# Kernel tuning notes

Hardware: AMD Instinct MI355X
Metric: run time of the kernel (lower is better)

The kernel has to match this reference:

```python
import jax, jax.numpy as jnp
import numpy as np

D_MODEL = 1024
N_HEADS = 16
D_K = D_MODEL // N_HEADS
B, N_Q, N_KV = 2, 2048, 2048


def setup_inputs() -> dict:
    key = jax.random.key(0)
    ks = jax.random.split(key, 13)
    s = 1.0 / np.sqrt(D_MODEL)
    Q = jax.random.normal(ks[0], (B, N_Q, D_MODEL), dtype=jnp.float32)
    K = jax.random.normal(ks[1], (B, N_KV, D_MODEL), dtype=jnp.float32)
    V = jax.random.normal(ks[2], (B, N_KV, D_MODEL), dtype=jnp.float32)
    mask = jax.random.uniform(ks[3], (B, N_KV)) > 0.1
    mask = mask.at[:, 0].set(True)  # ensure at least one valid kv per batch
    Wq = jax.random.uniform(ks[4], (D_MODEL, D_MODEL), minval=-s, maxval=s)
    bq = jax.random.uniform(ks[5], (D_MODEL,), minval=-s, maxval=s)
    Wk = jax.random.uniform(ks[6], (D_MODEL, D_MODEL), minval=-s, maxval=s)
    bk = jax.random.uniform(ks[7], (D_MODEL,), minval=-s, maxval=s)
    Wv = jax.random.uniform(ks[8], (D_MODEL, D_MODEL), minval=-s, maxval=s)
    bv = jax.random.uniform(ks[9], (D_MODEL,), minval=-s, maxval=s)
    Wo = jax.random.uniform(ks[10], (D_MODEL, D_MODEL), minval=-s, maxval=s)
    bo = jax.random.uniform(ks[11], (D_MODEL,), minval=-s, maxval=s)
    return {"Q": Q, "K": K, "V": V, "mask": mask,
            "Wq": Wq, "bq": bq, "Wk": Wk, "bk": bk,
            "Wv": Wv, "bv": bv, "Wo": Wo, "bo": bo}


def reference(Q, K, V, mask, Wq, bq, Wk, bk, Wv, bv, Wo, bo):
    Bsz, nq, _ = Q.shape
    nkv = K.shape[1]
    # torch Linear: y = x @ W.T + b
    q = (Q @ Wq.T + bq).reshape(Bsz, nq, N_HEADS, D_K).transpose(0, 2, 1, 3)
    k = (K @ Wk.T + bk).reshape(Bsz, nkv, N_HEADS, D_K).transpose(0, 2, 1, 3)
    v = (V @ Wv.T + bv).reshape(Bsz, nkv, N_HEADS, D_K).transpose(0, 2, 1, 3)
    scores = jnp.einsum('bhqd,bhkd->bhqk', q, k) / jnp.sqrt(jnp.float32(D_K))
    scores = jnp.where(mask[:, None, None, :], scores, -jnp.inf)
    attn = jax.nn.softmax(scores, axis=-1)  # dropout p=0 (eval) -> identity
    out = jnp.einsum('bhqk,bhkd->bhqd', attn, v)
    out = out.transpose(0, 2, 1, 3).reshape(Bsz, nq, D_MODEL)
    return (out @ Wo.T + bo, attn)
```

## Files before the change

### kernel.cpp

```cpp
#include <hip/hip_runtime.h>
#include <math.h>

#define H 16
#define DK 64
#define NSEQ 2048
#define DM 1024
#define BSZ 2

typedef float f32x4 __attribute__((ext_vector_type(4)));
typedef short bf16x8 __attribute__((ext_vector_type(8)));
typedef unsigned short u16;
typedef unsigned long long u64;

__device__ __forceinline__ u16 f2bf(float f) {
    unsigned int u = __float_as_uint(f);
    u += 0x7fffu + ((u >> 16) & 1u);
    return (u16)(u >> 16);
}
__device__ __forceinline__ float bf2f(u16 h) {
    return __uint_as_float(((unsigned int)h) << 16);
}
__device__ __forceinline__ unsigned f2fp8(float v) {
    unsigned u = __float_as_uint(v);
    unsigned r = u + 0x7FFFFu + ((u >> 20) & 1u);
    unsigned byte = ((r >> 20) - 0x3C0u) & 0x7Fu;
    return v == 0.f ? 0u : byte;
}
__device__ __forceinline__ float fp82f(unsigned b) {
    return b ? __uint_as_float((b + 0x3C0u) << 20) : 0.f;
}

__global__ __launch_bounds__(256)
void cvt4_bf16(const float* __restrict__ s0, const float* __restrict__ s1,
               const float* __restrict__ s2, const float* __restrict__ s3,
               u16* __restrict__ dst) {
    const int sel = blockIdx.x >> 10;
    const float* s = sel == 0 ? s0 : sel == 1 ? s1 : sel == 2 ? s2 : s3;
    const int i = ((blockIdx.x & 1023) * 256 + threadIdx.x) * 4;
    float4 v = *(const float4*)(&s[i]);
    ushort4 o = make_ushort4(f2bf(v.x), f2bf(v.y), f2bf(v.z), f2bf(v.w));
    *(ushort4*)(&dst[(size_t)sel * DM * DM + i]) = o;
}

__global__ __launch_bounds__(1024, 4)
void gemm_qkv(const float* __restrict__ Qs_, const float* __restrict__ Ks_,
              const float* __restrict__ Vs_,
              const u16* __restrict__ Wqb, const u16* __restrict__ Wkb,
              const u16* __restrict__ Wvb,
              const float* __restrict__ bq, const float* __restrict__ bk,
              const float* __restrict__ bv,
              u16* __restrict__ qd, u16* __restrict__ kd, u16* __restrict__ vt) {
    __shared__ __align__(16) u16 At[64 * 1024];

    const int which = blockIdx.x >> 6;
    const int mblk  = blockIdx.x & 63;
    const float* A    = which == 0 ? Qs_ : which == 1 ? Ks_ : Vs_;
    const u16*   Wb   = which == 0 ? Wqb : which == 1 ? Wkb : Wvb;
    const float* bias = which == 0 ? bq  : which == 1 ? bk  : bv;

    const int tid  = threadIdx.x;
    const int lane = tid & 63;
    const int w    = tid >> 6;
    const int m0   = mblk * 64;

    {
        const int row = tid & 63;
        const int kg  = tid >> 6;
#pragma unroll
        for (int i = 0; i < 8; ++i) {
            int k = kg * 64 + i * 8;
            float4 a0 = *(const float4*)(&A[(size_t)(m0 + row) * 1024 + k]);
            float4 a1 = *(const float4*)(&A[(size_t)(m0 + row) * 1024 + k + 4]);
            bf16x8 pv;
            pv[0] = (short)f2bf(a0.x); pv[1] = (short)f2bf(a0.y);
            pv[2] = (short)f2bf(a0.z); pv[3] = (short)f2bf(a0.w);
            pv[4] = (short)f2bf(a1.x); pv[5] = (short)f2bf(a1.y);
            pv[6] = (short)f2bf(a1.z); pv[7] = (short)f2bf(a1.w);
            int slot = (kg * 8 + i) ^ (row & 7);
            *(bf16x8*)(&At[row * 1024 + slot * 8]) = pv;
        }
    }
    __syncthreads();

    const int fr = lane & 15;
    const int fg = lane >> 4;

    f32x4 acc[4][4];
#pragma unroll
    for (int rf = 0; rf < 4; ++rf)
#pragma unroll
        for (int ct = 0; ct < 4; ++ct) acc[rf][ct] = {0.f, 0.f, 0.f, 0.f};

    const int nbase = w * 64;
    for (int ks = 0; ks < 32; ++ks) {
        int slot = (ks * 4 + fg) ^ (fr & 7);
        bf16x8 aA[4];
#pragma unroll
        for (int rf = 0; rf < 4; ++rf)
            aA[rf] = *(const bf16x8*)(&At[(rf * 16 + fr) * 1024 + slot * 8]);
#pragma unroll
        for (int ct = 0; ct < 4; ++ct) {
            bf16x8 bB = *(const bf16x8*)(&Wb[(size_t)(nbase + ct * 16 + fr) * 1024 + ks * 32 + fg * 8]);
#pragma unroll
            for (int rf = 0; rf < 4; ++rf)
                acc[rf][ct] = __builtin_amdgcn_mfma_f32_16x16x32_bf16(aA[rf], bB, acc[rf][ct], 0, 0, 0);
        }
    }

    const int b = m0 >> 11;
    if (which == 2) {
#pragma unroll
        for (int ct = 0; ct < 4; ++ct) {
            int n = nbase + ct * 16 + fr;
            float bvv = bias[n];
            int hh = n >> 6, d = n & 63;
            size_t base = ((size_t)(b * H + hh)) * DK * NSEQ + (size_t)d * NSEQ;
#pragma unroll
            for (int rf = 0; rf < 4; ++rf) {
                int kv = (m0 & 2047) + rf * 16 + fg * 4;
                ushort4 pk = make_ushort4(f2bf(acc[rf][ct][0] + bvv), f2bf(acc[rf][ct][1] + bvv),
                                          f2bf(acc[rf][ct][2] + bvv), f2bf(acc[rf][ct][3] + bvv));
                *(ushort4*)(&vt[base + kv]) = pk;
            }
        }
    } else {
        u16* C = which == 0 ? qd : kd;
#pragma unroll
        for (int ct = 0; ct < 4; ++ct) {
            int n = nbase + ct * 16 + fr;
            float bvv = bias[n];
            int hh = n >> 6, d = n & 63;
#pragma unroll
            for (int rf = 0; rf < 4; ++rf)
#pragma unroll
                for (int reg = 0; reg < 4; ++reg) {
                    int nq = (m0 & 2047) + rf * 16 + fg * 4 + reg;
                    C[(((size_t)(b * H + hh)) * NSEQ + nq) * DK + d] = f2bf(acc[rf][ct][reg] + bvv);
                }
        }
    }
}

__global__ __launch_bounds__(512)
void gemm_out(const u16* __restrict__ Ab, const u16* __restrict__ Wb,
              const float* __restrict__ bias, float* __restrict__ Cdst) {
    __shared__ __align__(16) char smem[32 * 1028 * 4];
    u16* At = (u16*)smem;

    const int tid  = threadIdx.x;
    const int lane = tid & 63;
    const int w    = tid >> 6;
    const int m0   = blockIdx.x * 32;

    {
        const int row = tid & 31;
        const int kg  = tid >> 5;
#pragma unroll
        for (int i = 0; i < 8; ++i) {
            int k = kg * 64 + i * 8;
            bf16x8 pv = *(const bf16x8*)(&Ab[(size_t)(m0 + row) * 1024 + k]);
            int slot = (kg * 8 + i) ^ (row & 7);
            *(bf16x8*)(&At[row * 1024 + slot * 8]) = pv;
        }
    }
    __syncthreads();

    const int fr = lane & 15;
    const int fg = lane >> 4;

    f32x4 acc[2][8];
#pragma unroll
    for (int rf = 0; rf < 2; ++rf)
#pragma unroll
        for (int ct = 0; ct < 8; ++ct) acc[rf][ct] = {0.f, 0.f, 0.f, 0.f};

    const int nbase = w * 128;
    for (int ks = 0; ks < 32; ++ks) {
        int slot = (ks * 4 + fg) ^ (fr & 7);
        bf16x8 aA0 = *(const bf16x8*)(&At[(fr     ) * 1024 + slot * 8]);
        bf16x8 aA1 = *(const bf16x8*)(&At[(16 + fr) * 1024 + slot * 8]);
#pragma unroll
        for (int ct = 0; ct < 8; ++ct) {
            bf16x8 bB = *(const bf16x8*)(&Wb[(size_t)(nbase + ct * 16 + fr) * 1024 + ks * 32 + fg * 8]);
            acc[0][ct] = __builtin_amdgcn_mfma_f32_16x16x32_bf16(aA0, bB, acc[0][ct], 0, 0, 0);
            acc[1][ct] = __builtin_amdgcn_mfma_f32_16x16x32_bf16(aA1, bB, acc[1][ct], 0, 0, 0);
        }
    }

    __syncthreads();
    float* Ct = (float*)smem;
#pragma unroll
    for (int ct = 0; ct < 8; ++ct) {
        int n = nbase + ct * 16 + fr;
        float bvv = bias[n];
#pragma unroll
        for (int rf = 0; rf < 2; ++rf)
#pragma unroll
            for (int reg = 0; reg < 4; ++reg)
                Ct[(rf * 16 + fg * 4 + reg) * 1028 + n] = acc[rf][ct][reg] + bvv;
    }
    __syncthreads();
#pragma unroll
    for (int rr = 0; rr < 4; ++rr) {
        int row = w * 4 + rr;
#pragma unroll
        for (int seg = 0; seg < 4; ++seg) {
            int c = seg * 256 + lane * 4;
            f32x4 v = *(const f32x4*)(&Ct[row * 1028 + c]);
            *(f32x4*)(&Cdst[(size_t)(m0 + row) * 1024 + c]) = v;
        }
    }
}

__global__ __launch_bounds__(512, 4)
void attn_mfma(const u16* __restrict__ qb, const u16* __restrict__ kb,
               const u16* __restrict__ vt, const int* __restrict__ mask,
               float* __restrict__ attn, u16* __restrict__ ao) {
    __shared__ __align__(16) unsigned char Pband[32][2056];
    __shared__ unsigned Mbits[64];
    __shared__ float Sws[8][32];
    __shared__ float Sinv[32];

    const int tid  = threadIdx.x;
    const int lane = tid & 63;
    const int w    = tid >> 6;
    const int fr   = lane & 15;
    const int fg   = lane >> 4;

    const int bid = blockIdx.x;
    const int wg  = (bid & 7) * 256 + (bid >> 3);
    const int bh  = wg >> 6;
    const int qt  = wg & 63;
    const int b   = bh / H, h = bh % H;
    const int q0  = qt * 32;

    const u16* qh = qb + (size_t)bh * NSEQ * DK;
    const u16* kh = kb + (size_t)bh * NSEQ * DK;
    const u16* vh = vt + (size_t)bh * DK * NSEQ;

#pragma unroll
    for (int j = 0; j < 4; ++j) {
        int kv = j * 512 + w * 64 + lane;
        unsigned long long bal = __ballot(mask[b * NSEQ + kv] != 0);
        if (lane == 0) {
            Mbits[j * 16 + w * 2]     = (unsigned)bal;
            Mbits[j * 16 + w * 2 + 1] = (unsigned)(bal >> 32);
        }
    }

    bf16x8 aQ[2][2];
#pragma unroll
    for (int qs = 0; qs < 2; ++qs)
#pragma unroll
        for (int ks = 0; ks < 2; ++ks)
            aQ[qs][ks] = *(const bf16x8*)(&qh[(size_t)(q0 + qs * 16 + fr) * DK + ks * 32 + fg * 8]);

    const int slab = w * 32;

    __syncthreads();

    float sum[2] = {0.f, 0.f};
    f32x4 accO[2][4];
#pragma unroll
    for (int qs = 0; qs < 2; ++qs)
#pragma unroll
        for (int g = 0; g < 4; ++g) accO[qs][g] = {0.f, 0.f, 0.f, 0.f};
    const float lscale = 0.125f * 1.44269504089f;

    const int kvbSel = fg >> 1;
    const int srcA   = ((fg & 1) * 2) * 16 + fr;
    const int srcB   = srcA + 16;

    for (int st = 0; st < 8; ++st) {
        const int cb = st * 256;

        bf16x8 bV[4];
#pragma unroll
        for (int g = 0; g < 4; ++g)
            bV[g] = *(const bf16x8*)(&vh[(size_t)(g * 16 + fr) * NSEQ + cb + slab + fg * 8]);

        bf16x8 aK[2][2];
#pragma unroll
        for (int kvb = 0; kvb < 2; ++kvb)
#pragma unroll
            for (int ks = 0; ks < 2; ++ks)
                aK[kvb][ks] = *(const bf16x8*)(&kh[(size_t)(cb + slab + kvb * 16 + fr) * DK + ks * 32 + fg * 8]);

        __builtin_amdgcn_s_setprio(1);
        f32x4 s[2][2];
#pragma unroll
        for (int qs = 0; qs < 2; ++qs)
#pragma unroll
            for (int kvb = 0; kvb < 2; ++kvb) {
                s[qs][kvb] = {0.f, 0.f, 0.f, 0.f};
#pragma unroll
                for (int ks = 0; ks < 2; ++ks)
                    s[qs][kvb] = __builtin_amdgcn_mfma_f32_16x16x32_bf16(aK[kvb][ks], aQ[qs][ks], s[qs][kvb], 0, 0, 0);
            }
        __builtin_amdgcn_s_setprio(0);

        const unsigned word = Mbits[st * 8 + w];
        u64 pkll[2][2];
#pragma unroll
        for (int qs = 0; qs < 2; ++qs)
#pragma unroll
            for (int kvb = 0; kvb < 2; ++kvb) {
                float e[4];
                unsigned p8 = 0;
                u64 pb = 0;
#pragma unroll
                for (int reg = 0; reg < 4; ++reg) {
                    bool mm = (word >> (kvb * 16 + fg * 4 + reg)) & 1u;
                    e[reg] = mm ? exp2f(s[qs][kvb][reg] * lscale) : 0.f;
                    sum[qs] += e[reg];
                    p8 |= f2fp8(e[reg]) << (reg * 8);
                    pb |= (u64)f2bf(e[reg]) << (reg * 16);
                }
                pkll[qs][kvb] = pb;
                *(unsigned*)(&Pband[qs * 16 + fr][cb + slab + kvb * 16 + fg * 4]) = p8;
            }

        __builtin_amdgcn_s_setprio(1);
#pragma unroll
        for (int qs = 0; qs < 2; ++qs) {
            u64 tA0 = (u64)__shfl((long long)pkll[qs][0], srcA);
            u64 tA1 = (u64)__shfl((long long)pkll[qs][1], srcA);
            u64 tB0 = (u64)__shfl((long long)pkll[qs][0], srcB);
            u64 tB1 = (u64)__shfl((long long)pkll[qs][1], srcB);
            u64 lo = kvbSel ? tA1 : tA0;
            u64 hi = kvbSel ? tB1 : tB0;
            bf16x8 aP;
#pragma unroll
            for (int j = 0; j < 4; ++j) {
                aP[j]     = (short)(u16)(lo >> (j * 16));
                aP[4 + j] = (short)(u16)(hi >> (j * 16));
            }
#pragma unroll
            for (int g = 0; g < 4; ++g)
                accO[qs][g] = __builtin_amdgcn_mfma_f32_16x16x32_bf16(aP, bV[g], accO[qs][g], 0, 0, 0);
        }
        __builtin_amdgcn_s_setprio(0);
    }

#pragma unroll
    for (int off = 16; off < 64; off <<= 1) {
#pragma unroll
        for (int qs = 0; qs < 2; ++qs)
            sum[qs] += __shfl_xor(sum[qs], off);
    }
    if (fg == 0) {
#pragma unroll
        for (int qs = 0; qs < 2; ++qs)
            Sws[w][qs * 16 + fr] = sum[qs];
    }
    __syncthreads();
    if (tid < 32) {
        float s = 0.f;
#pragma unroll
        for (int wv = 0; wv < 8; ++wv) s += Sws[wv][tid];
        Sinv[tid] = 1.0f / s;
    }
    __syncthreads();

#pragma unroll
    for (int rr = 0; rr < 4; ++rr) {
        int row = w * 4 + rr;
        float inv = Sinv[row];
        float* dst = attn + ((size_t)bh * NSEQ + q0 + row) * NSEQ;
#pragma unroll
        for (int seg = 0; seg < 8; ++seg) {
            int c = seg * 256 + lane * 4;
            unsigned wq = *(const unsigned*)(&Pband[row][c]);
            f32x4 o = { fp82f( wq        & 0xFFu) * inv,
                        fp82f((wq >>  8) & 0xFFu) * inv,
                        fp82f((wq >> 16) & 0xFFu) * inv,
                        fp82f((wq >> 24) & 0xFFu) * inv };
            __builtin_nontemporal_store(o, (f32x4*)(&dst[c]));
        }
    }

    asm volatile("s_waitcnt lgkmcnt(0)" ::: "memory");
    __builtin_amdgcn_sched_barrier(0);
    __builtin_amdgcn_s_barrier();

    float* Of = (float*)Pband;
#pragma unroll
    for (int qs = 0; qs < 2; ++qs)
#pragma unroll
        for (int g = 0; g < 4; ++g)
#pragma unroll
            for (int reg = 0; reg < 4; ++reg)
                Of[(w * 32 + qs * 16 + fg * 4 + reg) * 64 + g * 16 + fr] = accO[qs][g][reg];
    __syncthreads();
    {
        int row = tid >> 4, cq = (tid & 15) * 4;
        f32x4 o = {0.f, 0.f, 0.f, 0.f};
#pragma unroll
        for (int wv = 0; wv < 8; ++wv)
            o += *(const f32x4*)(&Of[(wv * 32 + row) * 64 + cq]);
        float inv = Sinv[row];
        ushort4 st4 = make_ushort4(f2bf(o[0] * inv), f2bf(o[1] * inv),
                                   f2bf(o[2] * inv), f2bf(o[3] * inv));
        *(ushort4*)(&ao[((size_t)(b * NSEQ + q0 + row)) * DM + h * DK + cq]) = st4;
    }
}

extern "C" void kernel_launch(void* const* d_in, const int* in_sizes, int n_in,
                              void* d_out, int out_size, void* d_ws, size_t ws_size,
                              hipStream_t stream) {
    const float* Q    = (const float*)d_in[0];
    const float* K    = (const float*)d_in[1];
    const float* V    = (const float*)d_in[2];
    const int*   mask = (const int*)  d_in[3];
    const float* Wq   = (const float*)d_in[4];
    const float* bq   = (const float*)d_in[5];
    const float* Wk   = (const float*)d_in[6];
    const float* bk   = (const float*)d_in[7];
    const float* Wv   = (const float*)d_in[8];
    const float* bv   = (const float*)d_in[9];
    const float* Wo   = (const float*)d_in[10];
    const float* bo   = (const float*)d_in[11];

    float* out  = (float*)d_out;
    float* attn = out + (size_t)BSZ * NSEQ * DM;

    u16* Wqb = (u16*)d_ws;
    u16* Wkb = Wqb + (size_t)DM * DM;
    u16* Wvb = Wkb + (size_t)DM * DM;
    u16* Wob = Wvb + (size_t)DM * DM;
    u16* qbp = Wob + (size_t)DM * DM;
    u16* kbp = qbp + (size_t)BSZ * NSEQ * DM;
    u16* vbp = kbp + (size_t)BSZ * NSEQ * DM;
    u16* aob = vbp + (size_t)BSZ * NSEQ * DM;
    u16* vtb = aob + (size_t)BSZ * NSEQ * DM;

    cvt4_bf16<<<dim3(4096), dim3(256), 0, stream>>>(Wq, Wk, Wv, Wo, Wqb);

    gemm_qkv<<<dim3(192), dim3(1024), 0, stream>>>(Q, K, V, Wqb, Wkb, Wvb,
                                                   bq, bk, bv, qbp, kbp, vtb);

    attn_mfma<<<dim3(BSZ * H * (NSEQ / 32)), dim3(512), 0, stream>>>(qbp, kbp, vtb, mask, attn, aob);

    gemm_out<<<dim3(BSZ * NSEQ / 32), dim3(512), 0, stream>>>(aob, Wob, bo, out);
}
```

Baseline: 310.3 us.

## Prefetch next K tile and stage P through LDS instead of shuffles

Loads K fragments for the next kv step ahead of time (register double-buffering) so global load latency overlaps compute. It replaces the cross-lane shuffles that rebuild the bf16 P operand with a small per-wave LDS staging buffer, written and read back after an lgkmcnt wait. The loop is also split per query sub-tile so the two sub-tiles interleave. In exchange it uses more registers for the prefetched K, adds LDS traffic and a full lgkmcnt wait, and reuses the Stag buffer across the qs iterations without a barrier, relying on in-wave ordering.

```diff
diff --git a/kernel.cpp b/kernel.cpp
--- a/kernel.cpp
+++ b/kernel.cpp
@@ -217,6 +217,7 @@
                const u16* __restrict__ vt, const int* __restrict__ mask,
                float* __restrict__ attn, u16* __restrict__ ao) {
     __shared__ __align__(16) unsigned char Pband[32][2056];
+    __shared__ __align__(16) u16 Stag[8][16][40];
     __shared__ unsigned Mbits[64];
     __shared__ float Sws[8][32];
     __shared__ float Sinv[32];
@@ -267,9 +268,12 @@
         for (int g = 0; g < 4; ++g) accO[qs][g] = {0.f, 0.f, 0.f, 0.f};
     const float lscale = 0.125f * 1.44269504089f;
 
-    const int kvbSel = fg >> 1;
-    const int srcA   = ((fg & 1) * 2) * 16 + fr;
-    const int srcB   = srcA + 16;
+    bf16x8 aKc[2][2];
+#pragma unroll
+    for (int kvb = 0; kvb < 2; ++kvb)
+#pragma unroll
+        for (int ks = 0; ks < 2; ++ks)
+            aKc[kvb][ks] = *(const bf16x8*)(&kh[(size_t)(slab + kvb * 16 + fr) * DK + ks * 32 + fg * 8]);
 
     for (int st = 0; st < 8; ++st) {
         const int cb = st * 256;
@@ -279,67 +283,59 @@
         for (int g = 0; g < 4; ++g)
             bV[g] = *(const bf16x8*)(&vh[(size_t)(g * 16 + fr) * NSEQ + cb + slab + fg * 8]);
 
-        bf16x8 aK[2][2];
+        const int stn = (st < 7) ? st + 1 : 7;
+        bf16x8 aKn[2][2];
 #pragma unroll
         for (int kvb = 0; kvb < 2; ++kvb)
 #pragma unroll
             for (int ks = 0; ks < 2; ++ks)
-                aK[kvb][ks] = *(const bf16x8*)(&kh[(size_t)(cb + slab + kvb * 16 + fr) * DK + ks * 32 + fg * 8]);
-
-        __builtin_amdgcn_s_setprio(1);
-        f32x4 s[2][2];
-#pragma unroll
-        for (int qs = 0; qs < 2; ++qs)
+                aKn[kvb][ks] = *(const bf16x8*)(&kh[(size_t)(stn * 256 + slab + kvb * 16 + fr) * DK + ks * 32 + fg * 8]);
+
+        const unsigned word = Mbits[st * 8 + w];
+
+#pragma unroll
+        for (int qs = 0; qs < 2; ++qs) {
+            __builtin_amdgcn_s_setprio(1);
+            f32x4 s[2];
 #pragma unroll
             for (int kvb = 0; kvb < 2; ++kvb) {
-                s[qs][kvb] = {0.f, 0.f, 0.f, 0.f};
+                s[kvb] = {0.f, 0.f, 0.f, 0.f};
 #pragma unroll
                 for (int ks = 0; ks < 2; ++ks)
-                    s[qs][kvb] = __builtin_amdgcn_mfma_f32_16x16x32_bf16(aK[kvb][ks], aQ[qs][ks], s[qs][kvb], 0, 0, 0);
+                    s[kvb] = __builtin_amdgcn_mfma_f32_16x16x32_bf16(aKc[kvb][ks], aQ[qs][ks], s[kvb], 0, 0, 0);
             }
-        __builtin_amdgcn_s_setprio(0);
-
-        const unsigned word = Mbits[st * 8 + w];
-        u64 pkll[2][2];
-#pragma unroll
-        for (int qs = 0; qs < 2; ++qs)
+            __builtin_amdgcn_s_setprio(0);
+
 #pragma unroll
             for (int kvb = 0; kvb < 2; ++kvb) {
                 float e[4];
                 unsigned p8 = 0;
-                u64 pb = 0;
 #pragma unroll
                 for (int reg = 0; reg < 4; ++reg) {
                     bool mm = (word >> (kvb * 16 + fg * 4 + reg)) & 1u;
-                    e[reg] = mm ? exp2f(s[qs][kvb][reg] * lscale) : 0.f;
+                    e[reg] = mm ? exp2f(s[kvb][reg] * lscale) : 0.f;
                     sum[qs] += e[reg];
                     p8 |= f2fp8(e[reg]) << (reg * 8);
-                    pb |= (u64)f2bf(e[reg]) << (reg * 16);
                 }
-                pkll[qs][kvb] = pb;
                 *(unsigned*)(&Pband[qs * 16 + fr][cb + slab + kvb * 16 + fg * 4]) = p8;
+                ushort4 pk = make_ushort4(f2bf(e[0]), f2bf(e[1]), f2bf(e[2]), f2bf(e[3]));
+                *(ushort4*)(&Stag[w][fr][kvb * 16 + fg * 4]) = pk;
             }
 
-        __builtin_amdgcn_s_setprio(1);
-#pragma unroll
-        for (int qs = 0; qs < 2; ++qs) {
-            u64 tA0 = (u64)__shfl((long long)pkll[qs][0], srcA);
-            u64 tA1 = (u64)__shfl((long long)pkll[qs][1], srcA);
-            u64 tB0 = (u64)__shfl((long long)pkll[qs][0], srcB);
-            u64 tB1 = (u64)__shfl((long long)pkll[qs][1], srcB);
-            u64 lo = kvbSel ? tA1 : tA0;
-            u64 hi = kvbSel ? tB1 : tB0;
-            bf16x8 aP;
-#pragma unroll
-            for (int j = 0; j < 4; ++j) {
-                aP[j]     = (short)(u16)(lo >> (j * 16));
-                aP[4 + j] = (short)(u16)(hi >> (j * 16));
-            }
+            asm volatile("s_waitcnt lgkmcnt(0)" ::: "memory");
+            bf16x8 aP = *(const bf16x8*)(&Stag[w][fr][fg * 8]);
+
+            __builtin_amdgcn_s_setprio(1);
 #pragma unroll
             for (int g = 0; g < 4; ++g)
                 accO[qs][g] = __builtin_amdgcn_mfma_f32_16x16x32_bf16(aP, bV[g], accO[qs][g], 0, 0, 0);
-        }
-        __builtin_amdgcn_s_setprio(0);
+            __builtin_amdgcn_s_setprio(0);
+        }
+
+#pragma unroll
+        for (int kvb = 0; kvb < 2; ++kvb)
+#pragma unroll
+            for (int ks = 0; ks < 2; ++ks) aKc[kvb][ks] = aKn[kvb][ks];
     }
 
 #pragma unroll
```

New measurement: 463.7 us. 49.4% more time.
